# Performance work log

Measured on AMD Instinct MI355X. Metric: run time of the kernel, lower is better.

## Reference

```python
import jax, jax.numpy as jnp
import numpy as np

HIDDEN = 128

def _lstm_final_h(xe, w_ih, w_hh, b_ih, b_hh):
    # xe: [B, T, E]. PyTorch gate order: i, f, g, o. Returns final h [B, H].
    B = xe.shape[0]
    bias = b_ih + b_hh  # [4H]
    # Precompute input projections for all timesteps: [T, B, 4H]
    gx = jnp.einsum('bte,ge->tbg', xe, w_ih) + bias
    h0 = jnp.zeros((B, HIDDEN), dtype=xe.dtype)
    c0 = jnp.zeros((B, HIDDEN), dtype=xe.dtype)

    def step(carry, gx_t):
        h, c = carry
        gates = gx_t + h @ w_hh.T  # [B, 4H]
        i, f, g, o = jnp.split(gates, 4, axis=-1)
        i = jax.nn.sigmoid(i)
        f = jax.nn.sigmoid(f)
        g = jnp.tanh(g)
        o = jax.nn.sigmoid(o)
        c = f * c + i * g
        h = o * jnp.tanh(c)
        return (h, c), None

    (h, _), _ = jax.lax.scan(step, (h0, c0), gx)
    return h

def setup_inputs() -> dict:
    key = jax.random.key(0)
    ks = jax.random.split(key, 8)
    V, E, H, C = 50257, 64, HIDDEN, 28
    B, T = 512, 1024
    s_ih = 1.0 / np.sqrt(H)
    return {
        'x': jax.random.randint(ks[0], (B, T), 0, V, dtype=jnp.int64),
        'emb_table': jax.random.normal(ks[1], (V, E), dtype=jnp.float32),
        'w_ih': jax.random.normal(ks[2], (4 * H, E), dtype=jnp.float32) * s_ih,
        'w_hh': jax.random.normal(ks[3], (4 * H, H), dtype=jnp.float32) * s_ih,
        'b_ih': jax.random.normal(ks[4], (4 * H,), dtype=jnp.float32) * s_ih,
        'b_hh': jax.random.normal(ks[5], (4 * H,), dtype=jnp.float32) * s_ih,
        'w_lin': jax.random.normal(ks[6], (C, H), dtype=jnp.float32) * s_ih,
        'b_lin': jax.random.normal(ks[7], (C,), dtype=jnp.float32) * s_ih,
    }

def reference(x, emb_table, w_ih, w_hh, b_ih, b_hh, w_lin, b_lin):
    xe = emb_table[x]  # [B, T, E]
    h = _lstm_final_h(xe, w_ih, w_hh, b_ih, b_hh)  # [B, H]
    return h @ w_lin.T + b_lin  # [B, 28]
```

## Files before the change

kernel.cpp:

```cpp
#include <hip/hip_runtime.h>

#define HID    128
#define GATES  512
#define EMB    64
#define TSTEPS 1024
#define BATCH  512
#define VOCAB  50257
#define NCLS   28
#define H8STRIDE 160
#define TPAD   8
#define TTAIL  4

#define S_SIG  (-1.442695041f)
#define S_TANH (-2.885390082f)

typedef __attribute__((ext_vector_type(8))) short short8;
typedef __attribute__((ext_vector_type(4))) float f32x4;
typedef __attribute__((ext_vector_type(4))) unsigned short us4;
typedef __attribute__((ext_vector_type(4))) int int4v;
typedef __attribute__((ext_vector_type(2))) int int2v;

#define BAR_LGKM() __asm__ __volatile__("s_waitcnt lgkmcnt(0)\n\ts_barrier" ::: "memory")

static __device__ __forceinline__ float bf2f(unsigned short u){
  union { unsigned int i; float f; } v; v.i = ((unsigned int)u) << 16; return v.f;
}
static __device__ __forceinline__ unsigned short f2bf(float f){
  union { float ff; unsigned int i; } v; v.ff = f;
  unsigned int x = v.i;
  x += 0x7fffu + ((x >> 16) & 1u);
  return (unsigned short)(x >> 16);
}

__global__ __launch_bounds__(256) void emb_proj_kernel(
    const float* __restrict__ emb,
    const float* __restrict__ w_ih,
    const float* __restrict__ b_ih,
    const float* __restrict__ b_hh,
    unsigned short* __restrict__ proj)
{
  int wave = threadIdx.x >> 6;
  int lane = threadIdx.x & 63;
  int n = lane & 15;
  int q = lane >> 4;
  long v0 = (long)blockIdx.x * 64;

  short8 bhi[4][2], blo[4][2];
  #pragma unroll
  for (int vt = 0; vt < 4; ++vt){
    long vrow = v0 + vt * 16 + n; if (vrow >= VOCAB) vrow = VOCAB - 1;
    const float* er = emb + vrow * EMB;
    #pragma unroll
    for (int ch = 0; ch < 2; ++ch){
      f32x4 e0 = *(const f32x4*)(er + ch * 32 + q * 8);
      f32x4 e1 = *(const f32x4*)(er + ch * 32 + q * 8 + 4);
      #pragma unroll
      for (int j = 0; j < 4; ++j){
        unsigned short h0 = f2bf(e0[j]);
        bhi[vt][ch][j] = (short)h0;
        blo[vt][ch][j] = (short)f2bf(e0[j] - bf2f(h0));
        unsigned short h1 = f2bf(e1[j]);
        bhi[vt][ch][j + 4] = (short)h1;
        blo[vt][ch][j + 4] = (short)f2bf(e1[j] - bf2f(h1));
      }
    }
  }

  #pragma unroll 1
  for (int i = 0; i < 8; ++i){
    int hc = (wave * 8 + i) * 4;
    const float* wr = w_ih + (long)((n & 3) * 128 + hc + (n >> 2)) * EMB;
    short8 ahi[2], alo[2];
    #pragma unroll
    for (int ch = 0; ch < 2; ++ch){
      f32x4 w0 = *(const f32x4*)(wr + ch * 32 + q * 8);
      f32x4 w1 = *(const f32x4*)(wr + ch * 32 + q * 8 + 4);
      #pragma unroll
      for (int j = 0; j < 4; ++j){
        unsigned short h0 = f2bf(w0[j]);
        ahi[ch][j] = (short)h0;
        alo[ch][j] = (short)f2bf(w0[j] - bf2f(h0));
        unsigned short h1 = f2bf(w1[j]);
        ahi[ch][j + 4] = (short)h1;
        alo[ch][j + 4] = (short)f2bf(w1[j] - bf2f(h1));
      }
    }
    f32x4 bias;
    #pragma unroll
    for (int r = 0; r < 4; ++r){
      int g = r * 128 + hc + q;
      bias[r] = b_ih[g] + b_hh[g];
    }
    #pragma unroll
    for (int vt = 0; vt < 4; ++vt){
      f32x4 acc = bias;
      #pragma unroll
      for (int ch = 0; ch < 2; ++ch){
        acc = __builtin_amdgcn_mfma_f32_16x16x32_bf16(ahi[ch], bhi[vt][ch], acc, 0, 0, 0);
        acc = __builtin_amdgcn_mfma_f32_16x16x32_bf16(ahi[ch], blo[vt][ch], acc, 0, 0, 0);
        acc = __builtin_amdgcn_mfma_f32_16x16x32_bf16(alo[ch], bhi[vt][ch], acc, 0, 0, 0);
      }
      long v = v0 + vt * 16 + n;
      if (v < VOCAB){
        us4 o;
        #pragma unroll
        for (int r = 0; r < 4; ++r)
          o[r] = f2bf(((r == 2) ? S_TANH : S_SIG) * acc[r]);
        *(us4*)(proj + v * GATES + (hc + q) * 4) = o;
      }
    }
  }
}

__global__ __launch_bounds__(512, 2) void lstm_kernel(
    const int* __restrict__ x,
    const float* __restrict__ w_hh,
    const unsigned short* __restrict__ proj,
    const float* __restrict__ w_lin,
    const float* __restrict__ b_lin,
    float* __restrict__ out)
{
  __shared__ int   tok_lds[2][TSTEPS + TPAD];
  __shared__ signed char h8[2][2][H8STRIDE];

  int tid  = threadIdx.x;
  int wave = tid >> 6;
  int lane = tid & 63;
  int n = lane & 15;
  int q = lane >> 4;
  int r0 = blockIdx.x * 2;

  for (int i = tid; i < TSTEPS + TTAIL; i += 512){
    int src = i < TSTEPS ? i : TSTEPS - 1;
    tok_lds[0][i] = x[(long)r0 * TSTEPS + src] * (GATES * 2);
    tok_lds[1][i] = x[(long)(r0 + 1) * TSTEPS + src] * (GATES * 2);
  }

  int4v Bw[4][2];
  float scl[4];
  #pragma unroll
  for (int t = 0; t < 4; ++t){
    int row = t * 128 + wave * 16 + n;
    const float* wr = w_hh + (long)row * HID;
    float vals[2][16];
    float m = 0.f;
    #pragma unroll
    for (int ch = 0; ch < 2; ++ch)
      #pragma unroll
      for (int j = 0; j < 16; ++j){
        float v = wr[ch * 64 + q * 16 + j];
        vals[ch][j] = v;
        m = fmaxf(m, fabsf(v));
      }
    m = fmaxf(m, __shfl_xor(m, 16, 64));
    m = fmaxf(m, __shfl_xor(m, 32, 64));
    m = fmaxf(m, 1e-20f);
    float qs = 127.f / m;
    #pragma unroll
    for (int ch = 0; ch < 2; ++ch){
      #pragma unroll
      for (int d = 0; d < 4; ++d){
        int b0 = (int)__builtin_rintf(vals[ch][d * 4 + 0] * qs);
        int b1 = (int)__builtin_rintf(vals[ch][d * 4 + 1] * qs);
        int b2 = (int)__builtin_rintf(vals[ch][d * 4 + 2] * qs);
        int b3 = (int)__builtin_rintf(vals[ch][d * 4 + 3] * qs);
        Bw[t][ch][d] = (b0 & 255) | ((b1 & 255) << 8) | ((b2 & 255) << 16) | (b3 << 24);
      }
    }
    scl[t] = ((t == 2) ? S_TANH : S_SIG) * m * (1.f / 16129.f);
  }

  for (int i = tid; i < 2 * 2 * H8STRIDE; i += 512) ((signed char*)h8)[i] = 0;

  float c_state = 0.f;
  int   arow  = (n >> 2) & 1;
  int   grow  = q & 1;
  int   hcol  = wave * 16 + n;

  const int4v ZERO4 = {0, 0, 0, 0};
  int ghcolB = hcol * 8;

  __syncthreads();

  us4 hxA, hxB;
  hxA = *(const us4*)((const char*)proj + (unsigned)(tok_lds[grow][0] + ghcolB));
  hxB = *(const us4*)((const char*)proj + (unsigned)(tok_lds[grow][1] + ghcolB));

#define SUBSTEP(RB, HX, TOKB)                                                 \
  {                                                                           \
    int4v Af0 = *(const int4v*)(&h8[RB][arow][q * 16]);                       \
    int4v Af1 = *(const int4v*)(&h8[RB][arow][64 + q * 16]);                  \
                                \
    float gx0 = bf2f(HX[0]), gx1 = bf2f(HX[1]);                               \
    float gx2 = bf2f(HX[2]), gx3 = bf2f(HX[3]);                               \
    HX = *(const us4*)((const char*)proj + (unsigned)((TOKB) + ghcolB));      \
                            \
    int4v a1 = __builtin_amdgcn_mfma_i32_16x16x64_i8(Af0, Bw[1][0], ZERO4, 0, 0, 0); \
    a1 = __builtin_amdgcn_mfma_i32_16x16x64_i8(Af1, Bw[1][1], a1, 0, 0, 0);   \
    float g1 = (float)a1[0] * scl[1] + gx1;                                   \
    float ef = __builtin_amdgcn_exp2f(g1);                                    \
    float sf = __builtin_amdgcn_rcpf(1.f + ef);                               \
    int4v a0 = __builtin_amdgcn_mfma_i32_16x16x64_i8(Af0, Bw[0][0], ZERO4, 0, 0, 0); \
    a0 = __builtin_amdgcn_mfma_i32_16x16x64_i8(Af1, Bw[0][1], a0, 0, 0, 0);   \
    float g0 = (float)a0[0] * scl[0] + gx0;                                   \
    float ei = __builtin_amdgcn_exp2f(g0);                                    \
    int4v a2 = __builtin_amdgcn_mfma_i32_16x16x64_i8(Af0, Bw[2][0], ZERO4, 0, 0, 0); \
    a2 = __builtin_amdgcn_mfma_i32_16x16x64_i8(Af1, Bw[2][1], a2, 0, 0, 0);   \
    float g2 = (float)a2[0] * scl[2] + gx2;                                   \
    float eg = __builtin_amdgcn_exp2f(fminf(g2, 126.f));                      \
    int4v a3 = __builtin_amdgcn_mfma_i32_16x16x64_i8(Af0, Bw[3][0], ZERO4, 0, 0, 0); \
    a3 = __builtin_amdgcn_mfma_i32_16x16x64_i8(Af1, Bw[3][1], a3, 0, 0, 0);   \
    float g3 = (float)a3[0] * scl[3] + gx3;                                   \
    float eo = __builtin_amdgcn_exp2f(g3);                                    \
    float r1 = __builtin_amdgcn_rcpf((1.f + ei) * (1.f + eg));                \
    float sitg = (1.f - eg) * r1;                                \
    c_state = sf * c_state + sitg;                                            \
    float ec = __builtin_amdgcn_exp2f(fminf(S_TANH * c_state, 126.f));        \
    float r2 = __builtin_amdgcn_rcpf((1.f + eo) * (1.f + ec));                \
    float hv = (1.f - ec) * r2;                             \
               \
    float qf = __builtin_fmaf(hv, 127.f, 12582912.f);                         \
    h8[(RB) ^ 1][grow][hcol] = (signed char)__float_as_uint(qf);              \
    BAR_LGKM();                                                               \
  }

  for (int step = 0; step < TSTEPS; step += 2){
    int2v tk = *(const int2v*)(&tok_lds[grow][step + 2]);
    SUBSTEP(0, hxA, tk[0])
    SUBSTEP(1, hxB, tk[1])
  }
#undef SUBSTEP

  if (tid < 2 * NCLS){
    int b = tid / NCLS, j = tid - b * NCLS;
    float s = 0.f;
    const float* wl = w_lin + (long)j * HID;
    #pragma unroll 4
    for (int k = 0; k < HID; ++k)
      s += (float)h8[0][b][k] * wl[k];
    out[(long)(r0 + b) * NCLS + j] = b_lin[j] + s * (1.f / 127.f);
  }
}

extern "C" void kernel_launch(void* const* d_in, const int* in_sizes, int n_in,
                              void* d_out, int out_size, void* d_ws, size_t ws_size,
                              hipStream_t stream)
{
  const int*   x     = (const int*)d_in[0];
  const float* emb   = (const float*)d_in[1];
  const float* w_ih  = (const float*)d_in[2];
  const float* w_hh  = (const float*)d_in[3];
  const float* b_ih  = (const float*)d_in[4];
  const float* b_hh  = (const float*)d_in[5];
  const float* w_lin = (const float*)d_in[6];
  const float* b_lin = (const float*)d_in[7];
  float*       out   = (float*)d_out;
  unsigned short* proj = (unsigned short*)d_ws;

  int vblocks = (VOCAB + 63) / 64;
  emb_proj_kernel<<<dim3(vblocks), dim3(256), 0, stream>>>(
      emb, w_ih, b_ih, b_hh, proj);
  lstm_kernel<<<dim3(BATCH / 2), dim3(512), 0, stream>>>(
      x, w_hh, proj, w_lin, b_lin, out);
}
```

Measured before the change: 442.8 us.

## Process one batch row per 4-wave block instead of two rows per 8-wave block

The LSTM recurrence kernel now launches one 256-thread block per batch row instead of one 512-thread block handling two rows. Each wave now owns 32 hidden columns: it holds twice as many quantized W_hh fragments and issues 16 int8 MFMAs per step, using lane-half selects to pick the right gate result. The aim is a cheaper per-step barrier across fewer waves and more independent blocks to schedule. The cost is a longer serial MFMA chain per wave on the recurrence critical path, plus MFMA work whose results are discarded by the selects.

```diff
diff --git a/kernel.cpp b/kernel.cpp
--- a/kernel.cpp
+++ b/kernel.cpp
@@ -112,7 +112,7 @@
   }
 }
 
-__global__ __launch_bounds__(512, 2) void lstm_kernel(
+__global__ __launch_bounds__(256, 2) void lstm_kernel(
     const int* __restrict__ x,
     const float* __restrict__ w_hh,
     const unsigned short* __restrict__ proj,
@@ -120,27 +120,27 @@
     const float* __restrict__ b_lin,
     float* __restrict__ out)
 {
-  __shared__ int   tok_lds[2][TSTEPS + TPAD];
-  __shared__ signed char h8[2][2][H8STRIDE];
+  __shared__ int   tok_lds[TSTEPS + TPAD];
+  __shared__ signed char h8[2][H8STRIDE];
 
   int tid  = threadIdx.x;
   int wave = tid >> 6;
   int lane = tid & 63;
   int n = lane & 15;
   int q = lane >> 4;
-  int r0 = blockIdx.x * 2;
-
-  for (int i = tid; i < TSTEPS + TTAIL; i += 512){
+  int r = blockIdx.x;
+
+  for (int i = tid; i < TSTEPS + TTAIL; i += 256){
     int src = i < TSTEPS ? i : TSTEPS - 1;
-    tok_lds[0][i] = x[(long)r0 * TSTEPS + src] * (GATES * 2);
-    tok_lds[1][i] = x[(long)(r0 + 1) * TSTEPS + src] * (GATES * 2);
-  }
-
-  int4v Bw[4][2];
-  float scl[4];
+    tok_lds[i] = x[(long)r * TSTEPS + src] * (GATES * 2);
+  }
+
+  int4v Bw[8][2];
+  float scl[8];
   #pragma unroll
-  for (int t = 0; t < 4; ++t){
-    int row = t * 128 + wave * 16 + n;
+  for (int t = 0; t < 8; ++t){
+    int type = t & 3, hgt = t >> 2;
+    int row = type * 128 + wave * 32 + hgt * 16 + n;
     const float* wr = w_hh + (long)row * HID;
     float vals[2][16];
     float m = 0.f;
@@ -167,50 +167,61 @@
         Bw[t][ch][d] = (b0 & 255) | ((b1 & 255) << 8) | ((b2 & 255) << 16) | (b3 << 24);
       }
     }
-    scl[t] = ((t == 2) ? S_TANH : S_SIG) * m * (1.f / 16129.f);
-  }
-
-  for (int i = tid; i < 2 * 2 * H8STRIDE; i += 512) ((signed char*)h8)[i] = 0;
+    scl[t] = ((type == 2) ? S_TANH : S_SIG) * m * (1.f / 16129.f);
+  }
+
+  int hg = (q >> 1) & 1;
+  float sclS0 = hg ? scl[4] : scl[0];
+  float sclS1 = hg ? scl[5] : scl[1];
+  float sclS2 = hg ? scl[6] : scl[2];
+  float sclS3 = hg ? scl[7] : scl[3];
+
+  for (int i = tid; i < 2 * H8STRIDE; i += 256) ((signed char*)h8)[i] = 0;
 
   float c_state = 0.f;
-  int   arow  = (n >> 2) & 1;
-  int   grow  = q & 1;
-  int   hcol  = wave * 16 + n;
-
+  int   hcol  = wave * 32 + hg * 16 + n;
   const int4v ZERO4 = {0, 0, 0, 0};
   int ghcolB = hcol * 8;
 
   __syncthreads();
 
   us4 hxA, hxB;
-  hxA = *(const us4*)((const char*)proj + (unsigned)(tok_lds[grow][0] + ghcolB));
-  hxB = *(const us4*)((const char*)proj + (unsigned)(tok_lds[grow][1] + ghcolB));
+  hxA = *(const us4*)((const char*)proj + (unsigned)(tok_lds[0] + ghcolB));
+  hxB = *(const us4*)((const char*)proj + (unsigned)(tok_lds[1] + ghcolB));
+
+#define MFMA8(AF0, AF1, T) \
+  (__builtin_amdgcn_mfma_i32_16x16x64_i8(AF0, Bw[T][0], ZERO4, 0, 0, 0)[0] + \
+   __builtin_amdgcn_mfma_i32_16x16x64_i8(AF1, Bw[T][1], ZERO4, 0, 0, 0)[0])
 
 #define SUBSTEP(RB, HX, TOKB)                                                 \
   {                                                                           \
-    int4v Af0 = *(const int4v*)(&h8[RB][arow][q * 16]);                       \
-    int4v Af1 = *(const int4v*)(&h8[RB][arow][64 + q * 16]);                  \
+    int4v Af0 = *(const int4v*)(&h8[RB][q * 16]);                             \
+    int4v Af1 = *(const int4v*)(&h8[RB][64 + q * 16]);                        \
                                 \
     float gx0 = bf2f(HX[0]), gx1 = bf2f(HX[1]);                               \
     float gx2 = bf2f(HX[2]), gx3 = bf2f(HX[3]);                               \
     HX = *(const us4*)((const char*)proj + (unsigned)((TOKB) + ghcolB));      \
-                            \
-    int4v a1 = __builtin_amdgcn_mfma_i32_16x16x64_i8(Af0, Bw[1][0], ZERO4, 0, 0, 0); \
-    a1 = __builtin_amdgcn_mfma_i32_16x16x64_i8(Af1, Bw[1][1], a1, 0, 0, 0);   \
-    float g1 = (float)a1[0] * scl[1] + gx1;                                   \
+                           \
+    int vf = hg ? MFMA8(Af0, Af1, 5) : 0;                                     \
+    int vf0 = hg ? 0 : MFMA8(Af0, Af1, 1);                                    \
+    vf += vf0;                                                                \
+    float g1 = (float)vf * sclS1 + gx1;                                       \
     float ef = __builtin_amdgcn_exp2f(g1);                                    \
     float sf = __builtin_amdgcn_rcpf(1.f + ef);                               \
-    int4v a0 = __builtin_amdgcn_mfma_i32_16x16x64_i8(Af0, Bw[0][0], ZERO4, 0, 0, 0); \
-    a0 = __builtin_amdgcn_mfma_i32_16x16x64_i8(Af1, Bw[0][1], a0, 0, 0, 0);   \
-    float g0 = (float)a0[0] * scl[0] + gx0;                                   \
+    int vi0 = MFMA8(Af0, Af1, 0);                                             \
+    int vi1 = MFMA8(Af0, Af1, 4);                                             \
+    int vi = hg ? vi1 : vi0;                                                  \
+    float g0 = (float)vi * sclS0 + gx0;                                       \
     float ei = __builtin_amdgcn_exp2f(g0);                                    \
-    int4v a2 = __builtin_amdgcn_mfma_i32_16x16x64_i8(Af0, Bw[2][0], ZERO4, 0, 0, 0); \
-    a2 = __builtin_amdgcn_mfma_i32_16x16x64_i8(Af1, Bw[2][1], a2, 0, 0, 0);   \
-    float g2 = (float)a2[0] * scl[2] + gx2;                                   \
+    int vg0 = MFMA8(Af0, Af1, 2);                                             \
+    int vg1 = MFMA8(Af0, Af1, 6);                                             \
+    int vg = hg ? vg1 : vg0;                                                  \
+    float g2 = (float)vg * sclS2 + gx2;                                       \
     float eg = __builtin_amdgcn_exp2f(fminf(g2, 126.f));                      \
-    int4v a3 = __builtin_amdgcn_mfma_i32_16x16x64_i8(Af0, Bw[3][0], ZERO4, 0, 0, 0); \
-    a3 = __builtin_amdgcn_mfma_i32_16x16x64_i8(Af1, Bw[3][1], a3, 0, 0, 0);   \
-    float g3 = (float)a3[0] * scl[3] + gx3;                                   \
+    int vo0 = MFMA8(Af0, Af1, 3);                                             \
+    int vo1 = MFMA8(Af0, Af1, 7);                                             \
+    int vo = hg ? vo1 : vo0;                                                  \
+    float g3 = (float)vo * sclS3 + gx3;                                       \
     float eo = __builtin_amdgcn_exp2f(g3);                                    \
     float r1 = __builtin_amdgcn_rcpf((1.f + ei) * (1.f + eg));                \
     float sitg = (1.f - eg) * r1;                                \
@@ -220,25 +231,25 @@
     float hv = (1.f - ec) * r2;                             \
                \
     float qf = __builtin_fmaf(hv, 127.f, 12582912.f);                         \
-    h8[(RB) ^ 1][grow][hcol] = (signed char)__float_as_uint(qf);              \
+    h8[(RB) ^ 1][hcol] = (signed char)__float_as_uint(qf);                    \
     BAR_LGKM();                                                               \
   }
 
   for (int step = 0; step < TSTEPS; step += 2){
-    int2v tk = *(const int2v*)(&tok_lds[grow][step + 2]);
+    int2v tk = *(const int2v*)(&tok_lds[step + 2]);
     SUBSTEP(0, hxA, tk[0])
     SUBSTEP(1, hxB, tk[1])
   }
 #undef SUBSTEP
-
-  if (tid < 2 * NCLS){
-    int b = tid / NCLS, j = tid - b * NCLS;
+#undef MFMA8
+
+  if (tid < NCLS){
     float s = 0.f;
-    const float* wl = w_lin + (long)j * HID;
+    const float* wl = w_lin + (long)tid * HID;
     #pragma unroll 4
     for (int k = 0; k < HID; ++k)
-      s += (float)h8[0][b][k] * wl[k];
-    out[(long)(r0 + b) * NCLS + j] = b_lin[j] + s * (1.f / 127.f);
+      s += (float)h8[0][k] * wl[k];
+    out[(long)r * NCLS + tid] = b_lin[tid] + s * (1.f / 127.f);
   }
 }
 
@@ -260,6 +271,6 @@
   int vblocks = (VOCAB + 63) / 64;
   emb_proj_kernel<<<dim3(vblocks), dim3(256), 0, stream>>>(
       emb, w_ih, b_ih, b_hh, proj);
-  lstm_kernel<<<dim3(BATCH / 2), dim3(512), 0, stream>>>(
+  lstm_kernel<<<dim3(BATCH), dim3(256), 0, stream>>>(
       x, w_hh, proj, w_lin, b_lin, out);
 }
```

Result: slower. 585.1 us (+32.1%).

## Halve LSTM block to 4 waves, each wave computing 32 hidden columns

Applied to the files above, without the earlier changes.

The recurrent kernel now runs 256 threads per block instead of 512. Each wave holds twice as many quantized W_hh tiles and issues 16 MFMAs per step covering 32 hidden columns, with lanes selecting their half by quadrant. The aim is cheaper per-step barriers across fewer waves and better MFMA pipelining from the independent accumulator pairs. In exchange each wave carries a longer serial chain per timestep and needs more registers. The launch bound also drops to one block per SIMD group.

```diff
diff --git a/kernel.cpp b/kernel.cpp
--- a/kernel.cpp
+++ b/kernel.cpp
@@ -112,7 +112,7 @@
   }
 }
 
-__global__ __launch_bounds__(512, 2) void lstm_kernel(
+__global__ __launch_bounds__(256, 1) void lstm_kernel(
     const int* __restrict__ x,
     const float* __restrict__ w_hh,
     const unsigned short* __restrict__ proj,
@@ -130,17 +130,18 @@
   int q = lane >> 4;
   int r0 = blockIdx.x * 2;
 
-  for (int i = tid; i < TSTEPS + TTAIL; i += 512){
+  for (int i = tid; i < TSTEPS + TTAIL; i += 256){
     int src = i < TSTEPS ? i : TSTEPS - 1;
     tok_lds[0][i] = x[(long)r0 * TSTEPS + src] * (GATES * 2);
     tok_lds[1][i] = x[(long)(r0 + 1) * TSTEPS + src] * (GATES * 2);
   }
 
-  int4v Bw[4][2];
-  float scl[4];
+  int4v Bw[8][2];
+  float sclA[8];
   #pragma unroll
-  for (int t = 0; t < 4; ++t){
-    int row = t * 128 + wave * 16 + n;
+  for (int t = 0; t < 8; ++t){
+    int type = t & 3, hgt = t >> 2;
+    int row = type * 128 + wave * 32 + hgt * 16 + n;
     const float* wr = w_hh + (long)row * HID;
     float vals[2][16];
     float m = 0.f;
@@ -167,16 +168,21 @@
         Bw[t][ch][d] = (b0 & 255) | ((b1 & 255) << 8) | ((b2 & 255) << 16) | (b3 << 24);
       }
     }
-    scl[t] = ((t == 2) ? S_TANH : S_SIG) * m * (1.f / 16129.f);
-  }
-
-  for (int i = tid; i < 2 * 2 * H8STRIDE; i += 512) ((signed char*)h8)[i] = 0;
+    sclA[t] = ((type == 2) ? S_TANH : S_SIG) * m * (1.f / 16129.f);
+  }
+
+  int hg   = q >> 1;
+  int grow = q & 1;
+  float sclS0 = hg ? sclA[4] : sclA[0];
+  float sclS1 = hg ? sclA[5] : sclA[1];
+  float sclS2 = hg ? sclA[6] : sclA[2];
+  float sclS3 = hg ? sclA[7] : sclA[3];
+
+  for (int i = tid; i < 2 * 2 * H8STRIDE; i += 256) ((signed char*)h8)[i] = 0;
 
   float c_state = 0.f;
   int   arow  = (n >> 2) & 1;
-  int   grow  = q & 1;
-  int   hcol  = wave * 16 + n;
-
+  int   hcol  = wave * 32 + hg * 16 + n;
   const int4v ZERO4 = {0, 0, 0, 0};
   int ghcolB = hcol * 8;
 
@@ -185,6 +191,8 @@
   us4 hxA, hxB;
   hxA = *(const us4*)((const char*)proj + (unsigned)(tok_lds[grow][0] + ghcolB));
   hxB = *(const us4*)((const char*)proj + (unsigned)(tok_lds[grow][1] + ghcolB));
+
+#define MFMA(A, B, C) __builtin_amdgcn_mfma_i32_16x16x64_i8(A, B, C, 0, 0, 0)
 
 #define SUBSTEP(RB, HX, TOKB)                                                 \
   {                                                                           \
@@ -194,23 +202,35 @@
     float gx0 = bf2f(HX[0]), gx1 = bf2f(HX[1]);                               \
     float gx2 = bf2f(HX[2]), gx3 = bf2f(HX[3]);                               \
     HX = *(const us4*)((const char*)proj + (unsigned)((TOKB) + ghcolB));      \
-                            \
-    int4v a1 = __builtin_amdgcn_mfma_i32_16x16x64_i8(Af0, Bw[1][0], ZERO4, 0, 0, 0); \
-    a1 = __builtin_amdgcn_mfma_i32_16x16x64_i8(Af1, Bw[1][1], a1, 0, 0, 0);   \
-    float g1 = (float)a1[0] * scl[1] + gx1;                                   \
+      \
+    int4v F0 = MFMA(Af0, Bw[1][0], ZERO4);                                    \
+    int4v F1 = MFMA(Af0, Bw[5][0], ZERO4);                                    \
+    F0 = MFMA(Af1, Bw[1][1], F0);                                             \
+    F1 = MFMA(Af1, Bw[5][1], F1);                                             \
+    int4v I0 = MFMA(Af0, Bw[0][0], ZERO4);                                    \
+    int4v I1 = MFMA(Af0, Bw[4][0], ZERO4);                                    \
+    I0 = MFMA(Af1, Bw[0][1], I0);                                             \
+    I1 = MFMA(Af1, Bw[4][1], I1);                                             \
+    int vf = hg ? F1[0] : F0[0];                                              \
+    float g1 = __builtin_fmaf((float)vf, sclS1, gx1);                         \
     float ef = __builtin_amdgcn_exp2f(g1);                                    \
     float sf = __builtin_amdgcn_rcpf(1.f + ef);                               \
-    int4v a0 = __builtin_amdgcn_mfma_i32_16x16x64_i8(Af0, Bw[0][0], ZERO4, 0, 0, 0); \
-    a0 = __builtin_amdgcn_mfma_i32_16x16x64_i8(Af1, Bw[0][1], a0, 0, 0, 0);   \
-    float g0 = (float)a0[0] * scl[0] + gx0;                                   \
+    int4v G0 = MFMA(Af0, Bw[2][0], ZERO4);                                    \
+    int4v G1 = MFMA(Af0, Bw[6][0], ZERO4);                                    \
+    G0 = MFMA(Af1, Bw[2][1], G0);                                             \
+    G1 = MFMA(Af1, Bw[6][1], G1);                                             \
+    int vi = hg ? I1[0] : I0[0];                                              \
+    float g0 = __builtin_fmaf((float)vi, sclS0, gx0);                         \
     float ei = __builtin_amdgcn_exp2f(g0);                                    \
-    int4v a2 = __builtin_amdgcn_mfma_i32_16x16x64_i8(Af0, Bw[2][0], ZERO4, 0, 0, 0); \
-    a2 = __builtin_amdgcn_mfma_i32_16x16x64_i8(Af1, Bw[2][1], a2, 0, 0, 0);   \
-    float g2 = (float)a2[0] * scl[2] + gx2;                                   \
+    int4v O0 = MFMA(Af0, Bw[3][0], ZERO4);                                    \
+    int4v O1 = MFMA(Af0, Bw[7][0], ZERO4);                                    \
+    O0 = MFMA(Af1, Bw[3][1], O0);                                             \
+    O1 = MFMA(Af1, Bw[7][1], O1);                                             \
+    int vg = hg ? G1[0] : G0[0];                                              \
+    float g2 = __builtin_fmaf((float)vg, sclS2, gx2);                         \
     float eg = __builtin_amdgcn_exp2f(fminf(g2, 126.f));                      \
-    int4v a3 = __builtin_amdgcn_mfma_i32_16x16x64_i8(Af0, Bw[3][0], ZERO4, 0, 0, 0); \
-    a3 = __builtin_amdgcn_mfma_i32_16x16x64_i8(Af1, Bw[3][1], a3, 0, 0, 0);   \
-    float g3 = (float)a3[0] * scl[3] + gx3;                                   \
+    int vo = hg ? O1[0] : O0[0];                                              \
+    float g3 = __builtin_fmaf((float)vo, sclS3, gx3);                         \
     float eo = __builtin_amdgcn_exp2f(g3);                                    \
     float r1 = __builtin_amdgcn_rcpf((1.f + ei) * (1.f + eg));                \
     float sitg = (1.f - eg) * r1;                                \
@@ -230,6 +250,7 @@
     SUBSTEP(1, hxB, tk[1])
   }
 #undef SUBSTEP
+#undef MFMA
 
   if (tid < 2 * NCLS){
     int b = tid / NCLS, j = tid - b * NCLS;
@@ -260,6 +281,6 @@
   int vblocks = (VOCAB + 63) / 64;
   emb_proj_kernel<<<dim3(vblocks), dim3(256), 0, stream>>>(
       emb, w_ih, b_ih, b_hh, proj);
-  lstm_kernel<<<dim3(BATCH / 2), dim3(512), 0, stream>>>(
+  lstm_kernel<<<dim3(BATCH / 2), dim3(256), 0, stream>>>(
       x, w_hh, proj, w_lin, b_lin, out);
 }
```

Result: faster. 398.8 us (-9.9%).
